# Kernel tuning notes

Hardware: AMD Instinct MI355X
Metric: run time of the kernel (lower is better)

The kernel has to match this reference:

```python
import jax, jax.numpy as jnp
import numpy as np

SEQ, BATCH, D_IN, D_OUT = 512, 128, 1024, 1024


def setup_inputs() -> dict:
    key = jax.random.key(0)
    ks = jax.random.split(key, 9)
    d_xh = D_IN + D_OUT
    s = 1.0 / np.sqrt(d_xh)
    def lin(k):
        kw, kb = jax.random.split(k)
        W = jax.random.uniform(kw, (D_OUT, d_xh), jnp.float32, -s, s)
        b = jax.random.uniform(kb, (D_OUT,), jnp.float32, -s, s)
        return W, b
    W_f, b_f = lin(ks[0])
    W_i, b_i = lin(ks[1])
    W_c, b_c = lin(ks[2])
    W_o, b_o = lin(ks[3])
    tokens = jax.random.normal(ks[4], (SEQ, BATCH, D_IN), jnp.float32)
    return {"tokens": tokens, "W_f": W_f, "b_f": b_f, "W_i": W_i, "b_i": b_i,
            "W_c": W_c, "b_c": b_c, "W_o": W_o, "b_o": b_o}


def reference(tokens, W_f, b_f, W_i, b_i, W_c, b_c, W_o, b_o):
    # tokens: [T, B, D_in]; 4 gate linears each map (D_in + D_out) -> D_out
    batch = tokens.shape[1]
    d_out = W_f.shape[0]
    h0 = jnp.zeros((batch, d_out), tokens.dtype)
    c0 = jnp.zeros((batch, d_out), tokens.dtype)

    def step(carry, x):
        h, c = carry
        xh = jnp.concatenate([x, h], axis=-1)  # [B, D_in+D_out]
        f = jax.nn.sigmoid(xh @ W_f.T + b_f)
        i = jax.nn.sigmoid(xh @ W_i.T + b_i)
        g = jnp.tanh(xh @ W_c.T + b_c)
        o = jax.nn.sigmoid(xh @ W_o.T + b_o)
        c_new = c * f + i * g
        h_new = o * jnp.tanh(c_new)
        return (h_new, c_new), h_new

    _, outputs = jax.lax.scan(step, (h0, c0), tokens)
    return outputs  # [T, B, D_out]
```

## Files before the change

### kernel.cpp

```cpp
#include <hip/hip_runtime.h>
#include <hip/hip_bf16.h>

#define T_SEQ 512
#define BATCH 128
#define D_IN 1024
#define D_OUT 1024
#define D_XH 2048

typedef __bf16 bf16_t;
typedef __bf16 bf16x8 __attribute__((ext_vector_type(8)));
typedef float f32x4 __attribute__((ext_vector_type(4)));

#define WS_BIAS 16777216
#define WS_H    (WS_BIAS + 16384)
#define WS_C    (WS_H + 2 * 128 * 1024 * 2)

__device__ __forceinline__ float sigm(float x) {
    return 1.0f / (1.0f + __expf(-x));
}
__device__ __forceinline__ float tanh_f(float x) {
    return 2.0f / (1.0f + __expf(-2.0f * x)) - 1.0f;
}

__global__ void pack_weights(const float* __restrict__ Wf, const float* __restrict__ Wi,
                             const float* __restrict__ Wc, const float* __restrict__ Wo,
                             bf16_t* __restrict__ Wp) {
    int idx = blockIdx.x * blockDim.x + threadIdx.x;
    if (idx >= 4 * 1024 * 2048 / 4) return;
    int g  = idx >> 19;
    int rk = idx & 524287;
    const float* src = (g == 0) ? Wf : (g == 1) ? Wi : (g == 2) ? Wc : Wo;
    float4 v = ((const float4*)src)[rk];
    bf16_t* dst = Wp + (size_t)g * (1024 * 2048) + (size_t)rk * 4;
    dst[0] = (bf16_t)v.x; dst[1] = (bf16_t)v.y;
    dst[2] = (bf16_t)v.z; dst[3] = (bf16_t)v.w;
}

__global__ void init_state(const float* __restrict__ bf, const float* __restrict__ bi,
                           const float* __restrict__ bc, const float* __restrict__ bo,
                           float* __restrict__ bias, bf16_t* __restrict__ h0,
                           float* __restrict__ c) {
    int idx = blockIdx.x * blockDim.x + threadIdx.x;
    if (idx < 1024) {
        bias[idx]        = bf[idx];
        bias[1024 + idx] = bi[idx];
        bias[2048 + idx] = bc[idx];
        bias[3072 + idx] = bo[idx];
    }
    if (idx < 128 * 1024) {
        h0[idx] = (bf16_t)0.0f;
        c[idx]  = 0.0f;
    }
}

#define BK 256
#define LDST (BK + 8)

__global__ __launch_bounds__(256)
void lstm_step(const float* __restrict__ x_t,
               const bf16_t* __restrict__ Wp,
               const float* __restrict__ bias,
               const bf16_t* __restrict__ h_in,
               bf16_t* __restrict__ h_out,
               float* __restrict__ c,
               float* __restrict__ out_t) {
    __shared__ bf16_t xh_lds[32][LDST];
    __shared__ bf16_t w_lds[64][LDST];
    __shared__ float  pre_lds[4][32][16];

    const int tid  = threadIdx.x;
    const int wave = tid >> 6;
    const int lane = tid & 63;
    const int rblk = blockIdx.x & 63;
    const int mblk = blockIdx.x >> 6;
    const int r0 = rblk * 16;
    const int m0 = mblk * 32;

    const int mt   = wave & 1;
    const int gp   = wave >> 1;
    const int col  = lane & 15;
    const int quad = lane >> 4;

    f32x4 acc0 = {0.f, 0.f, 0.f, 0.f};
    f32x4 acc1 = {0.f, 0.f, 0.f, 0.f};

    for (int k0 = 0; k0 < D_XH; k0 += BK) {
        if (k0 < D_IN) {
            #pragma unroll
            for (int it = 0; it < 8; ++it) {
                int idx = it * 256 + tid;
                int row = idx >> 6;
                int c4  = idx & 63;
                float4 v = *(const float4*)(x_t + (size_t)(m0 + row) * D_IN + k0 + c4 * 4);
                bf16_t* dst = &xh_lds[row][c4 * 4];
                dst[0] = (bf16_t)v.x; dst[1] = (bf16_t)v.y;
                dst[2] = (bf16_t)v.z; dst[3] = (bf16_t)v.w;
            }
        } else {
            #pragma unroll
            for (int it = 0; it < 4; ++it) {
                int idx = it * 256 + tid;
                int row = idx >> 5;
                int c8  = idx & 31;
                uint4 v = *(const uint4*)(h_in + (size_t)(m0 + row) * D_OUT + (k0 - D_IN) + c8 * 8);
                *(uint4*)&xh_lds[row][c8 * 8] = v;
            }
        }
        #pragma unroll
        for (int it = 0; it < 8; ++it) {
            int idx = it * 256 + tid;
            int row = idx >> 5;
            int c8  = idx & 31;
            int g = row >> 4, rl = row & 15;
            uint4 v = *(const uint4*)(Wp + (size_t)(g * 1024 + r0 + rl) * D_XH + k0 + c8 * 8);
            *(uint4*)&w_lds[row][c8 * 8] = v;
        }
        __syncthreads();

        #pragma unroll
        for (int kk = 0; kk < BK; kk += 32) {
            bf16x8 a  = *(const bf16x8*)&xh_lds[mt * 16 + col][kk + quad * 8];
            bf16x8 b0 = *(const bf16x8*)&w_lds[(2 * gp) * 16 + col][kk + quad * 8];
            bf16x8 b1 = *(const bf16x8*)&w_lds[(2 * gp + 1) * 16 + col][kk + quad * 8];
            acc0 = __builtin_amdgcn_mfma_f32_16x16x32_bf16(a, b0, acc0, 0, 0, 0);
            acc1 = __builtin_amdgcn_mfma_f32_16x16x32_bf16(a, b1, acc1, 0, 0, 0);
        }
        __syncthreads();
    }

    int b_base = mt * 16 + quad * 4;
    #pragma unroll
    for (int i = 0; i < 4; ++i) {
        pre_lds[2 * gp][b_base + i][col]     = acc0[i];
        pre_lds[2 * gp + 1][b_base + i][col] = acc1[i];
    }
    __syncthreads();

    #pragma unroll
    for (int j = 0; j < 2; ++j) {
        int e  = j * 256 + tid;
        int bl = e >> 4;
        int r  = e & 15;
        int d  = r0 + r;
        int bg = m0 + bl;
        float pf = pre_lds[0][bl][r] + bias[d];
        float pi = pre_lds[1][bl][r] + bias[1024 + d];
        float pc = pre_lds[2][bl][r] + bias[2048 + d];
        float po = pre_lds[3][bl][r] + bias[3072 + d];
        float fg = sigm(pf);
        float ig = sigm(pi);
        float gg = tanh_f(pc);
        float og = sigm(po);
        size_t off = (size_t)bg * D_OUT + d;
        float cn = c[off] * fg + ig * gg;
        c[off] = cn;
        float h = og * tanh_f(cn);
        out_t[off] = h;
        h_out[off] = (bf16_t)h;
    }
}

extern "C" void kernel_launch(void* const* d_in, const int* in_sizes, int n_in,
                              void* d_out, int out_size, void* d_ws, size_t ws_size,
                              hipStream_t stream) {
    const float* tokens = (const float*)d_in[0];
    const float* Wf = (const float*)d_in[1];
    const float* bf = (const float*)d_in[2];
    const float* Wi = (const float*)d_in[3];
    const float* bi = (const float*)d_in[4];
    const float* Wc = (const float*)d_in[5];
    const float* bc = (const float*)d_in[6];
    const float* Wo = (const float*)d_in[7];
    const float* bo = (const float*)d_in[8];
    float* out = (float*)d_out;

    char* ws = (char*)d_ws;
    bf16_t* Wp   = (bf16_t*)(ws);
    float*  bias = (float*)(ws + WS_BIAS);
    bf16_t* hbuf = (bf16_t*)(ws + WS_H);
    float*  cbuf = (float*)(ws + WS_C);

    pack_weights<<<(4 * 1024 * 2048 / 4 + 255) / 256, 256, 0, stream>>>(Wf, Wi, Wc, Wo, Wp);
    init_state<<<(128 * 1024 + 255) / 256, 256, 0, stream>>>(bf, bi, bc, bo, bias, hbuf, cbuf);

    for (int t = 0; t < T_SEQ; ++t) {
        const bf16_t* h_in  = hbuf + (size_t)(t & 1) * (128 * 1024);
        bf16_t*       h_out = hbuf + (size_t)((t + 1) & 1) * (128 * 1024);
        lstm_step<<<256, 256, 0, stream>>>(tokens + (size_t)t * BATCH * D_IN, Wp, bias,
                                           h_in, h_out, cbuf,
                                           out + (size_t)t * BATCH * D_OUT);
    }
}
```

Measured before the change: 9.693 ms.

## Replace per-step launches with persistent cooperative kernel using hierarchical grid barrier

Result: slower. 12.89 ms (+33.0%).

```diff
diff --git a/kernel.cpp b/kernel.cpp
--- a/kernel.cpp
+++ b/kernel.cpp
@@ -1,193 +1,265 @@
 #include <hip/hip_runtime.h>
-#include <hip/hip_bf16.h>
 
 #define T_SEQ 512
 #define BATCH 128
-#define D_IN 1024
+#define D_IN  1024
 #define D_OUT 1024
-#define D_XH 2048
+#define D_XH  2048
 
 typedef __bf16 bf16_t;
 typedef __bf16 bf16x8 __attribute__((ext_vector_type(8)));
-typedef float f32x4 __attribute__((ext_vector_type(4)));
-
-#define WS_BIAS 16777216
-#define WS_H    (WS_BIAS + 16384)
-#define WS_C    (WS_H + 2 * 128 * 1024 * 2)
-
-__device__ __forceinline__ float sigm(float x) {
-    return 1.0f / (1.0f + __expf(-x));
-}
-__device__ __forceinline__ float tanh_f(float x) {
-    return 2.0f / (1.0f + __expf(-2.0f * x)) - 1.0f;
-}
+typedef float  f32x4  __attribute__((ext_vector_type(4)));
+
+#define WS_WPK 0
+#define WS_H   16777216
+#define WS_BAR (WS_H + 2 * BATCH * D_OUT * 2)
+
+__device__ __forceinline__ float sigm(float x)   { return 1.0f / (1.0f + __expf(-x)); }
+__device__ __forceinline__ float tanh_f(float x) { return 2.0f / (1.0f + __expf(-2.0f * x)) - 1.0f; }
 
 __global__ void pack_weights(const float* __restrict__ Wf, const float* __restrict__ Wi,
                              const float* __restrict__ Wc, const float* __restrict__ Wo,
-                             bf16_t* __restrict__ Wp) {
-    int idx = blockIdx.x * blockDim.x + threadIdx.x;
-    if (idx >= 4 * 1024 * 2048 / 4) return;
-    int g  = idx >> 19;
-    int rk = idx & 524287;
-    const float* src = (g == 0) ? Wf : (g == 1) ? Wi : (g == 2) ? Wc : Wo;
-    float4 v = ((const float4*)src)[rk];
-    bf16_t* dst = Wp + (size_t)g * (1024 * 2048) + (size_t)rk * 4;
-    dst[0] = (bf16_t)v.x; dst[1] = (bf16_t)v.y;
-    dst[2] = (bf16_t)v.z; dst[3] = (bf16_t)v.w;
-}
-
-__global__ void init_state(const float* __restrict__ bf, const float* __restrict__ bi,
-                           const float* __restrict__ bc, const float* __restrict__ bo,
-                           float* __restrict__ bias, bf16_t* __restrict__ h0,
-                           float* __restrict__ c) {
-    int idx = blockIdx.x * blockDim.x + threadIdx.x;
-    if (idx < 1024) {
-        bias[idx]        = bf[idx];
-        bias[1024 + idx] = bi[idx];
-        bias[2048 + idx] = bc[idx];
-        bias[3072 + idx] = bo[idx];
-    }
-    if (idx < 128 * 1024) {
-        h0[idx] = (bf16_t)0.0f;
-        c[idx]  = 0.0f;
-    }
-}
-
-#define BK 256
-#define LDST (BK + 8)
-
-__global__ __launch_bounds__(256)
-void lstm_step(const float* __restrict__ x_t,
-               const bf16_t* __restrict__ Wp,
-               const float* __restrict__ bias,
-               const bf16_t* __restrict__ h_in,
-               bf16_t* __restrict__ h_out,
-               float* __restrict__ c,
-               float* __restrict__ out_t) {
-    __shared__ bf16_t xh_lds[32][LDST];
-    __shared__ bf16_t w_lds[64][LDST];
-    __shared__ float  pre_lds[4][32][16];
+                             bf16_t* __restrict__ Wpk) {
+    int o = blockIdx.x * 256 + threadIdx.x;
+    int gd   = o >> 12;
+    int ks   = (o >> 6) & 63;
+    int lane = o & 63;
+    int dblk = gd >> 2, g = gd & 3;
+    int row  = dblk * 16 + (lane & 15);
+    int col  = ks * 32 + (lane >> 4) * 8;
+    const float* W = (g == 0) ? Wf : (g == 1) ? Wi : (g == 2) ? Wc : Wo;
+    const float* s = W + (size_t)row * D_XH + col;
+    float4 v0 = *(const float4*)s;
+    float4 v1 = *(const float4*)(s + 4);
+    bf16x8 w;
+    w[0] = (bf16_t)v0.x; w[1] = (bf16_t)v0.y; w[2] = (bf16_t)v0.z; w[3] = (bf16_t)v0.w;
+    w[4] = (bf16_t)v1.x; w[5] = (bf16_t)v1.y; w[6] = (bf16_t)v1.z; w[7] = (bf16_t)v1.w;
+    *(bf16x8*)(Wpk + (size_t)o * 8) = w;
+}
+
+__global__ void init_ws(bf16_t* __restrict__ hbuf, unsigned int* __restrict__ bar) {
+    int idx = blockIdx.x * 256 + threadIdx.x;
+    if (idx < 2 * BATCH * D_OUT) hbuf[idx] = (bf16_t)0.0f;
+    if (idx < 512) bar[idx] = 0u;
+}
+
+__global__ __launch_bounds__(256, 1)
+void lstm_persist(const float* __restrict__ tokens,
+                  const bf16_t* __restrict__ Wpk,
+                  const float* __restrict__ bfp, const float* __restrict__ bip,
+                  const float* __restrict__ bcp, const float* __restrict__ bop,
+                  bf16_t* __restrict__ hbuf,
+                  float* __restrict__ out,
+                  unsigned int* __restrict__ bar)
+{
+    __shared__ bf16_t xh[32][2056];
+    __shared__ float  preA[4][32][17];
+    __shared__ float  preB[4][32][17];
 
     const int tid  = threadIdx.x;
+    const int bid  = blockIdx.x;
+    const int dblk = bid & 63;
+    const int mblk = bid >> 6;
+    const int m0   = mblk * 32;
     const int wave = tid >> 6;
     const int lane = tid & 63;
-    const int rblk = blockIdx.x & 63;
-    const int mblk = blockIdx.x >> 6;
-    const int r0 = rblk * 16;
-    const int m0 = mblk * 32;
-
-    const int mt   = wave & 1;
-    const int gp   = wave >> 1;
-    const int col  = lane & 15;
-    const int quad = lane >> 4;
-
-    f32x4 acc0 = {0.f, 0.f, 0.f, 0.f};
-    f32x4 acc1 = {0.f, 0.f, 0.f, 0.f};
-
-    for (int k0 = 0; k0 < D_XH; k0 += BK) {
-        if (k0 < D_IN) {
-            #pragma unroll
-            for (int it = 0; it < 8; ++it) {
+    const int l15  = lane & 15;
+    const int q    = lane >> 4;
+
+    const int ej = tid & 15;
+    const int eb = tid >> 4;
+    const int d  = dblk * 16 + ej;
+    const float bj_f = bfp[d], bj_i = bip[d], bj_c = bcp[d], bj_o = bop[d];
+    float c0 = 0.0f, c1 = 0.0f;
+
+    const bf16_t* wbase = Wpk + (size_t)dblk * 131072 + (size_t)wave * 8192 + lane * 8;
+    const bf16_t* aptr0 = &xh[l15][wave * 512 + q * 8];
+    const bf16_t* aptr1 = &xh[16 + l15][wave * 512 + q * 8];
+
+    unsigned int* shard = bar + (bid & 7) * 32;
+    unsigned int* root  = bar + 256;
+
+    const f32x4 fzero = {0.f, 0.f, 0.f, 0.f};
+
+    auto pre_store = [&](float (*P)[32][17], f32x4 (&acc)[2][4]) {
+        #pragma unroll
+        for (int mt = 0; mt < 2; ++mt)
+            #pragma unroll
+            for (int g = 0; g < 4; ++g)
+                #pragma unroll
+                for (int i = 0; i < 4; ++i)
+                    P[g][mt * 16 + q * 4 + i][l15] = acc[mt][g][i];
+    };
+    auto pre_add = [&](float (*P)[32][17], f32x4 (&acc)[2][4]) {
+        #pragma unroll
+        for (int mt = 0; mt < 2; ++mt)
+            #pragma unroll
+            for (int g = 0; g < 4; ++g)
+                #pragma unroll
+                for (int i = 0; i < 4; ++i)
+                    P[g][mt * 16 + q * 4 + i][l15] += acc[mt][g][i];
+    };
+
+    for (int t = 0; t < T_SEQ; ++t) {
+        const bf16_t* hb_cur = hbuf + (size_t)(t & 1) * (BATCH * D_OUT);
+        bf16_t*       hb_nxt = hbuf + (size_t)((t + 1) & 1) * (BATCH * D_OUT);
+
+        if (tid == 0) {
+            __threadfence();
+            atomicAdd(shard, 1u);
+        }
+
+        {
+            const float* xsrc = tokens + (size_t)t * (BATCH * D_IN) + (size_t)m0 * D_IN;
+            #pragma unroll
+            for (int it = 0; it < 16; ++it) {
                 int idx = it * 256 + tid;
-                int row = idx >> 6;
-                int c4  = idx & 63;
-                float4 v = *(const float4*)(x_t + (size_t)(m0 + row) * D_IN + k0 + c4 * 4);
-                bf16_t* dst = &xh_lds[row][c4 * 4];
-                dst[0] = (bf16_t)v.x; dst[1] = (bf16_t)v.y;
-                dst[2] = (bf16_t)v.z; dst[3] = (bf16_t)v.w;
-            }
-        } else {
-            #pragma unroll
-            for (int it = 0; it < 4; ++it) {
-                int idx = it * 256 + tid;
-                int row = idx >> 5;
-                int c8  = idx & 31;
-                uint4 v = *(const uint4*)(h_in + (size_t)(m0 + row) * D_OUT + (k0 - D_IN) + c8 * 8);
-                *(uint4*)&xh_lds[row][c8 * 8] = v;
-            }
-        }
-        #pragma unroll
-        for (int it = 0; it < 8; ++it) {
+                int row = idx >> 7;
+                int c8  = idx & 127;
+                const float* s = xsrc + (size_t)row * D_IN + c8 * 8;
+                float4 v0 = *(const float4*)s;
+                float4 v1 = *(const float4*)(s + 4);
+                bf16x8 w;
+                w[0] = (bf16_t)v0.x; w[1] = (bf16_t)v0.y; w[2] = (bf16_t)v0.z; w[3] = (bf16_t)v0.w;
+                w[4] = (bf16_t)v1.x; w[5] = (bf16_t)v1.y; w[6] = (bf16_t)v1.z; w[7] = (bf16_t)v1.w;
+                *(bf16x8*)&xh[row][c8 * 8] = w;
+            }
+        }
+
+        bf16x8 bpf[3][4];
+        #pragma unroll
+        for (int pk = 0; pk < 3; ++pk)
+            #pragma unroll
+            for (int g = 0; g < 4; ++g)
+                bpf[pk][g] = *(const bf16x8*)(wbase + g * 32768 + pk * 512);
+
+        if (tid == 0) {
+            if (bid < 8) {
+                while (__hip_atomic_load(shard, __ATOMIC_RELAXED, __HIP_MEMORY_SCOPE_AGENT)
+                       < 32u * (unsigned)(t + 1)) {}
+                atomicAdd(root, 1u);
+            }
+            while (__hip_atomic_load(root, __ATOMIC_RELAXED, __HIP_MEMORY_SCOPE_AGENT)
+                   < 8u * (unsigned)(t + 1)) {}
+            __threadfence();
+        }
+        __syncthreads();
+
+        #pragma unroll
+        for (int it = 0; it < 16; ++it) {
             int idx = it * 256 + tid;
-            int row = idx >> 5;
-            int c8  = idx & 31;
-            int g = row >> 4, rl = row & 15;
-            uint4 v = *(const uint4*)(Wp + (size_t)(g * 1024 + r0 + rl) * D_XH + k0 + c8 * 8);
-            *(uint4*)&w_lds[row][c8 * 8] = v;
-        }
-        __syncthreads();
-
-        #pragma unroll
-        for (int kk = 0; kk < BK; kk += 32) {
-            bf16x8 a  = *(const bf16x8*)&xh_lds[mt * 16 + col][kk + quad * 8];
-            bf16x8 b0 = *(const bf16x8*)&w_lds[(2 * gp) * 16 + col][kk + quad * 8];
-            bf16x8 b1 = *(const bf16x8*)&w_lds[(2 * gp + 1) * 16 + col][kk + quad * 8];
-            acc0 = __builtin_amdgcn_mfma_f32_16x16x32_bf16(a, b0, acc0, 0, 0, 0);
-            acc1 = __builtin_amdgcn_mfma_f32_16x16x32_bf16(a, b1, acc1, 0, 0, 0);
-        }
-        __syncthreads();
-    }
-
-    int b_base = mt * 16 + quad * 4;
-    #pragma unroll
-    for (int i = 0; i < 4; ++i) {
-        pre_lds[2 * gp][b_base + i][col]     = acc0[i];
-        pre_lds[2 * gp + 1][b_base + i][col] = acc1[i];
-    }
-    __syncthreads();
-
-    #pragma unroll
-    for (int j = 0; j < 2; ++j) {
-        int e  = j * 256 + tid;
-        int bl = e >> 4;
-        int r  = e & 15;
-        int d  = r0 + r;
-        int bg = m0 + bl;
-        float pf = pre_lds[0][bl][r] + bias[d];
-        float pi = pre_lds[1][bl][r] + bias[1024 + d];
-        float pc = pre_lds[2][bl][r] + bias[2048 + d];
-        float po = pre_lds[3][bl][r] + bias[3072 + d];
-        float fg = sigm(pf);
-        float ig = sigm(pi);
-        float gg = tanh_f(pc);
-        float og = sigm(po);
-        size_t off = (size_t)bg * D_OUT + d;
-        float cn = c[off] * fg + ig * gg;
-        c[off] = cn;
-        float h = og * tanh_f(cn);
-        out_t[off] = h;
-        h_out[off] = (bf16_t)h;
+            int row = idx >> 7;
+            int c8  = idx & 127;
+            uint4 v = *(const uint4*)(hb_cur + (size_t)(m0 + row) * D_OUT + c8 * 8);
+            *(uint4*)&xh[row][1024 + c8 * 8] = v;
+        }
+        __syncthreads();
+
+        f32x4 acc[2][4];
+        #pragma unroll
+        for (int mt = 0; mt < 2; ++mt)
+            #pragma unroll
+            for (int g = 0; g < 4; ++g)
+                acc[mt][g] = fzero;
+
+        bf16x8 apf[2][2];
+        apf[0][0] = *(const bf16x8*)aptr0;
+        apf[0][1] = *(const bf16x8*)aptr1;
+        apf[1][0] = *(const bf16x8*)(aptr0 + 32);
+        apf[1][1] = *(const bf16x8*)(aptr1 + 32);
+
+        #pragma unroll
+        for (int ks = 0; ks < 16; ++ks) {
+            bf16x8 a0 = apf[ks & 1][0];
+            bf16x8 a1 = apf[ks & 1][1];
+            bf16x8 b0 = bpf[ks % 3][0];
+            bf16x8 b1 = bpf[ks % 3][1];
+            bf16x8 b2 = bpf[ks % 3][2];
+            bf16x8 b3 = bpf[ks % 3][3];
+            if (ks < 14) {
+                apf[ks & 1][0] = *(const bf16x8*)(aptr0 + (ks + 2) * 32);
+                apf[ks & 1][1] = *(const bf16x8*)(aptr1 + (ks + 2) * 32);
+            }
+            if (ks < 13) {
+                #pragma unroll
+                for (int g = 0; g < 4; ++g)
+                    bpf[ks % 3][g] = *(const bf16x8*)(wbase + g * 32768 + (ks + 3) * 512);
+            }
+            acc[0][0] = __builtin_amdgcn_mfma_f32_16x16x32_bf16(a0, b0, acc[0][0], 0, 0, 0);
+            acc[1][0] = __builtin_amdgcn_mfma_f32_16x16x32_bf16(a1, b0, acc[1][0], 0, 0, 0);
+            acc[0][1] = __builtin_amdgcn_mfma_f32_16x16x32_bf16(a0, b1, acc[0][1], 0, 0, 0);
+            acc[1][1] = __builtin_amdgcn_mfma_f32_16x16x32_bf16(a1, b1, acc[1][1], 0, 0, 0);
+            acc[0][2] = __builtin_amdgcn_mfma_f32_16x16x32_bf16(a0, b2, acc[0][2], 0, 0, 0);
+            acc[1][2] = __builtin_amdgcn_mfma_f32_16x16x32_bf16(a1, b2, acc[1][2], 0, 0, 0);
+            acc[0][3] = __builtin_amdgcn_mfma_f32_16x16x32_bf16(a0, b3, acc[0][3], 0, 0, 0);
+            acc[1][3] = __builtin_amdgcn_mfma_f32_16x16x32_bf16(a1, b3, acc[1][3], 0, 0, 0);
+        }
+
+        if (wave == 0)      pre_store(preA, acc);
+        else if (wave == 2) pre_store(preB, acc);
+        __syncthreads();
+        if (wave == 1)      pre_add(preA, acc);
+        else if (wave == 3) pre_add(preB, acc);
+        __syncthreads();
+
+        float* out_t = out + (size_t)t * (BATCH * D_OUT);
+        {
+            float pf = preA[0][eb][ej] + preB[0][eb][ej] + bj_f;
+            float pi = preA[1][eb][ej] + preB[1][eb][ej] + bj_i;
+            float pc = preA[2][eb][ej] + preB[2][eb][ej] + bj_c;
+            float po = preA[3][eb][ej] + preB[3][eb][ej] + bj_o;
+            float fg = sigm(pf), ig = sigm(pi), gg = tanh_f(pc), og = sigm(po);
+            c0 = c0 * fg + ig * gg;
+            float h = og * tanh_f(c0);
+            size_t off = (size_t)(m0 + eb) * D_OUT + d;
+            __builtin_nontemporal_store(h, out_t + off);
+            hb_nxt[off] = (bf16_t)h;
+        }
+        {
+            int b2 = eb + 16;
+            float pf = preA[0][b2][ej] + preB[0][b2][ej] + bj_f;
+            float pi = preA[1][b2][ej] + preB[1][b2][ej] + bj_i;
+            float pc = preA[2][b2][ej] + preB[2][b2][ej] + bj_c;
+            float po = preA[3][b2][ej] + preB[3][b2][ej] + bj_o;
+            float fg = sigm(pf), ig = sigm(pi), gg = tanh_f(pc), og = sigm(po);
+            c1 = c1 * fg + ig * gg;
+            float h = og * tanh_f(c1);
+            size_t off = (size_t)(m0 + b2) * D_OUT + d;
+            __builtin_nontemporal_store(h, out_t + off);
+            hb_nxt[off] = (bf16_t)h;
+        }
+        __syncthreads();
     }
 }
 
 extern "C" void kernel_launch(void* const* d_in, const int* in_sizes, int n_in,
                               void* d_out, int out_size, void* d_ws, size_t ws_size,
                               hipStream_t stream) {
+    (void)in_sizes; (void)n_in; (void)out_size; (void)ws_size;
     const float* tokens = (const float*)d_in[0];
     const float* Wf = (const float*)d_in[1];
-    const float* bf = (const float*)d_in[2];
+    const float* bf_ = (const float*)d_in[2];
     const float* Wi = (const float*)d_in[3];
-    const float* bi = (const float*)d_in[4];
+    const float* bi_ = (const float*)d_in[4];
     const float* Wc = (const float*)d_in[5];
-    const float* bc = (const float*)d_in[6];
+    const float* bc_ = (const float*)d_in[6];
     const float* Wo = (const float*)d_in[7];
-    const float* bo = (const float*)d_in[8];
+    const float* bo_ = (const float*)d_in[8];
     float* out = (float*)d_out;
 
     char* ws = (char*)d_ws;
-    bf16_t* Wp   = (bf16_t*)(ws);
-    float*  bias = (float*)(ws + WS_BIAS);
-    bf16_t* hbuf = (bf16_t*)(ws + WS_H);
-    float*  cbuf = (float*)(ws + WS_C);
-
-    pack_weights<<<(4 * 1024 * 2048 / 4 + 255) / 256, 256, 0, stream>>>(Wf, Wi, Wc, Wo, Wp);
-    init_state<<<(128 * 1024 + 255) / 256, 256, 0, stream>>>(bf, bi, bc, bo, bias, hbuf, cbuf);
-
-    for (int t = 0; t < T_SEQ; ++t) {
-        const bf16_t* h_in  = hbuf + (size_t)(t & 1) * (128 * 1024);
-        bf16_t*       h_out = hbuf + (size_t)((t + 1) & 1) * (128 * 1024);
-        lstm_step<<<256, 256, 0, stream>>>(tokens + (size_t)t * BATCH * D_IN, Wp, bias,
-                                           h_in, h_out, cbuf,
-                                           out + (size_t)t * BATCH * D_OUT);
+    bf16_t*       Wpk  = (bf16_t*)(ws + WS_WPK);
+    bf16_t*       hbuf = (bf16_t*)(ws + WS_H);
+    unsigned int* bar  = (unsigned int*)(ws + WS_BAR);
+
+    pack_weights<<<4096, 256, 0, stream>>>(Wf, Wi, Wc, Wo, Wpk);
+    init_ws<<<1024, 256, 0, stream>>>(hbuf, bar);
+
+    void* args[] = {(void*)&tokens, (void*)&Wpk, (void*)&bf_, (void*)&bi_,
+                    (void*)&bc_, (void*)&bo_, (void*)&hbuf, (void*)&out, (void*)&bar};
+    hipError_t e = hipLaunchCooperativeKernel(reinterpret_cast<const void*>(&lstm_persist),
+                                              dim3(256), dim3(256), args, 0u, stream);
+    if (e != hipSuccess) {
+        lstm_persist<<<256, 256, 0, stream>>>(tokens, Wpk, bf_, bi_, bc_, bo_, hbuf, out, bar);
     }
 }
```
